# Optimization experiments

Hardware: AMD Instinct MI355X
Metric: run time of the kernel (lower is better)

The kernel has to match this reference:

```python
import jax, jax.numpy as jnp
import numpy as np

N = 8192
COUP = 0.08
ALPHA = 0.45
DT = 0.01
DIFF = 10.0


def setup_inputs() -> dict:
    key = jax.random.key(0)
    k1, k2, k3 = jax.random.split(key, 3)
    phase = jax.random.normal(k1, (N,), dtype=jnp.float32)
    w = jax.random.uniform(k2, (N,), dtype=jnp.float32) * (2.0 * np.pi * 1.5)
    xy = jax.random.normal(k3, (N, 2), dtype=jnp.float32) * 0.05
    xy_dot_old = jnp.zeros((N, 2), dtype=jnp.float32)
    return {"phase": phase, "w": w, "xy": xy, "xy_dot_old": xy_dot_old}


def reference(phase, w, xy, xy_dot_old):
    n = xy.shape[0]
    x = xy[:, 0]
    y = xy[:, 1]

    # per-edge rotation R(d_ij) with d_ij = phase_i - phase_j; diagonal d_ii = 0 -> R = I
    d = phase[:, None] - phase[None, :]            # (n, n)
    c = jnp.cos(d)
    s = jnp.sin(d)

    # sum_j R_ij @ xy_j over ALL j (diagonal contributes identity * xy_i),
    # then remove the self term since adjacency excludes i == j.
    sum_x = c @ x - s @ y                          # (n,)
    sum_y = s @ x + c @ y
    inv_deg = 1.0 / (n - 1)
    coup_x = COUP * (sum_x - x) * inv_deg
    coup_y = COUP * (sum_y - y) * inv_deg

    # local Hopf-like dynamics
    r2 = x * x + y * y
    a = ALPHA * (1.0 - r2)
    xdot = a * x - w * y + coup_x
    ydot = w * x + a * y + coup_y

    # slew-rate clamp to old derivative +/- DIFF
    xdot = jnp.clip(xdot, xy_dot_old[:, 0] - DIFF, xy_dot_old[:, 0] + DIFF)
    ydot = jnp.clip(ydot, xy_dot_old[:, 1] - DIFF, xy_dot_old[:, 1] + DIFF)

    new_xyd = jnp.stack([xdot, ydot], axis=-1)     # (n, 2)
    new_xy = xy + DT * new_xyd                     # (n, 2)
    y_unit = jnp.clip(new_xy[:, 1], -1.0, 1.0)     # unit outputs in [-1, 1]
    return new_xy, new_xyd, y_unit
```

## Files before the change

kernel.cpp:

```cpp
#include <hip/hip_runtime.h>
#include <math.h>


#define NOSC 8192
#define NTHREADS 1024
#define PER_THREAD (NOSC / NTHREADS)

__global__ __launch_bounds__(NTHREADS, 1) void nacpg_kernel(
    const float* __restrict__ phase,
    const float* __restrict__ w,
    const float* __restrict__ xy,
    const float* __restrict__ xy_dot_old,
    float* __restrict__ out)
{
    constexpr float COUP  = 0.08f;
    constexpr float ALPHA = 0.45f;
    constexpr float DT    = 0.01f;
    constexpr float DIFF  = 10.0f;

    const int tid = threadIdx.x;

    float c[PER_THREAD], s[PER_THREAD], x[PER_THREAD], y[PER_THREAD];
    float sA = 0.f, sB = 0.f, sC = 0.f, sD = 0.f;

    #pragma unroll
    for (int k = 0; k < PER_THREAD; ++k) {
        const int i = tid + k * NTHREADS;
        const float p = phase[i];
        const float2 v = reinterpret_cast<const float2*>(xy)[i];
        x[k] = v.x; y[k] = v.y;
        float ss, cc;
        sincosf(p, &ss, &cc);
        c[k] = cc; s[k] = ss;
        sA = fmaf(cc, v.x, sA);
        sB = fmaf(ss, v.x, sB);
        sC = fmaf(cc, v.y, sC);
        sD = fmaf(ss, v.y, sD);
    }

    #pragma unroll
    for (int off = 32; off >= 1; off >>= 1) {
        sA += __shfl_xor(sA, off);
        sB += __shfl_xor(sB, off);
        sC += __shfl_xor(sC, off);
        sD += __shfl_xor(sD, off);
    }

    __shared__ float red[4][NTHREADS / 64];
    const int wave = tid >> 6;
    const int lane = tid & 63;
    if (lane == 0) {
        red[0][wave] = sA; red[1][wave] = sB;
        red[2][wave] = sC; red[3][wave] = sD;
    }
    __syncthreads();

    float A = 0.f, B = 0.f, C = 0.f, D = 0.f;
    #pragma unroll
    for (int wv = 0; wv < NTHREADS / 64; ++wv) {
        A += red[0][wv]; B += red[1][wv];
        C += red[2][wv]; D += red[3][wv];
    }

    const float AD = A + D;
    const float BC = B - C;
    const float CB = C - B;
    const float inv_deg = 1.0f / (float)(NOSC - 1);

    float2* __restrict__ out_xy  = reinterpret_cast<float2*>(out);
    float2* __restrict__ out_xyd = reinterpret_cast<float2*>(out + 2 * NOSC);
    float*  __restrict__ out_yu  = out + 4 * NOSC;

    #pragma unroll
    for (int k = 0; k < PER_THREAD; ++k) {
        const int i = tid + k * NTHREADS;
        const float ci = c[k], si = s[k];
        const float xi = x[k], yi = y[k];

        const float sum_x = ci * AD + si * BC;
        const float sum_y = si * AD + ci * CB;
        const float coup_x = COUP * (sum_x - xi) * inv_deg;
        const float coup_y = COUP * (sum_y - yi) * inv_deg;

        const float r2 = xi * xi + yi * yi;
        const float a  = ALPHA * (1.0f - r2);
        const float wi = w[i];

        float xdot = a * xi - wi * yi + coup_x;
        float ydot = wi * xi + a * yi + coup_y;

        const float2 old = reinterpret_cast<const float2*>(xy_dot_old)[i];
        xdot = fminf(fmaxf(xdot, old.x - DIFF), old.x + DIFF);
        ydot = fminf(fmaxf(ydot, old.y - DIFF), old.y + DIFF);

        const float nx = xi + DT * xdot;
        const float ny = yi + DT * ydot;

        out_xy[i]  = make_float2(nx, ny);
        out_xyd[i] = make_float2(xdot, ydot);
        out_yu[i]  = fminf(fmaxf(ny, -1.0f), 1.0f);
    }
}

extern "C" void kernel_launch(void* const* d_in, const int* in_sizes, int n_in,
                              void* d_out, int out_size, void* d_ws, size_t ws_size,
                              hipStream_t stream) {
    const float* phase      = (const float*)d_in[0];
    const float* w          = (const float*)d_in[1];
    const float* xy         = (const float*)d_in[2];
    const float* xy_dot_old = (const float*)d_in[3];
    float* out = (float*)d_out;

    nacpg_kernel<<<1, NTHREADS, 0, stream>>>(phase, w, xy, xy_dot_old, out);
}
```

Baseline: 64.79 us.

## Split into two multi-block kernels with workspace partial sums and fast sincos

Replaces the single 1024-thread block with two launches of 64 blocks each. The first kernel computes per-block partial sums of cos/sin-weighted x and y into workspace. The second kernel reduces the 64 partials in every wave and computes the per-oscillator update. It also switches to the fast __sincosf intrinsic, which can lose accuracy for large phase arguments, and adds a second launch's overhead.

```diff
diff --git a/kernel.cpp b/kernel.cpp
--- a/kernel.cpp
+++ b/kernel.cpp
@@ -3,14 +3,50 @@
 
 
 #define NOSC 8192
-#define NTHREADS 1024
-#define PER_THREAD (NOSC / NTHREADS)
+#define NTHR 128
+#define NBLK (NOSC / NTHR)
 
-__global__ __launch_bounds__(NTHREADS, 1) void nacpg_kernel(
+__global__ __launch_bounds__(NTHR, 1) void nacpg_partial(
+    const float* __restrict__ phase,
+    const float* __restrict__ xy,
+    float4* __restrict__ part)
+{
+    const int i = blockIdx.x * NTHR + threadIdx.x;
+    const float p = phase[i];
+    const float2 v = reinterpret_cast<const float2*>(xy)[i];
+    float s, c;
+    __sincosf(p, &s, &c);
+
+    float A = c * v.x;
+    float B = s * v.x;
+    float C = c * v.y;
+    float D = s * v.y;
+
+    #pragma unroll
+    for (int off = 32; off >= 1; off >>= 1) {
+        A += __shfl_xor(A, off);
+        B += __shfl_xor(B, off);
+        C += __shfl_xor(C, off);
+        D += __shfl_xor(D, off);
+    }
+
+    __shared__ float4 red[NTHR / 64];
+    const int wave = threadIdx.x >> 6;
+    const int lane = threadIdx.x & 63;
+    if (lane == 0) red[wave] = make_float4(A, B, C, D);
+    __syncthreads();
+    if (threadIdx.x == 0) {
+        float4 a = red[0], b = red[1];
+        part[blockIdx.x] = make_float4(a.x + b.x, a.y + b.y, a.z + b.z, a.w + b.w);
+    }
+}
+
+__global__ __launch_bounds__(NTHR, 1) void nacpg_main(
     const float* __restrict__ phase,
     const float* __restrict__ w,
     const float* __restrict__ xy,
     const float* __restrict__ xy_dot_old,
+    const float4* __restrict__ part,
     float* __restrict__ out)
 {
     constexpr float COUP  = 0.08f;
@@ -18,48 +54,22 @@
     constexpr float DT    = 0.01f;
     constexpr float DIFF  = 10.0f;
 
-    const int tid = threadIdx.x;
+    const int i    = blockIdx.x * NTHR + threadIdx.x;
+    const int lane = threadIdx.x & 63;
 
-    float c[PER_THREAD], s[PER_THREAD], x[PER_THREAD], y[PER_THREAD];
-    float sA = 0.f, sB = 0.f, sC = 0.f, sD = 0.f;
+    const float p       = phase[i];
+    const float wi      = w[i];
+    const float2 v      = reinterpret_cast<const float2*>(xy)[i];
+    const float2 old    = reinterpret_cast<const float2*>(xy_dot_old)[i];
 
-    #pragma unroll
-    for (int k = 0; k < PER_THREAD; ++k) {
-        const int i = tid + k * NTHREADS;
-        const float p = phase[i];
-        const float2 v = reinterpret_cast<const float2*>(xy)[i];
-        x[k] = v.x; y[k] = v.y;
-        float ss, cc;
-        sincosf(p, &ss, &cc);
-        c[k] = cc; s[k] = ss;
-        sA = fmaf(cc, v.x, sA);
-        sB = fmaf(ss, v.x, sB);
-        sC = fmaf(cc, v.y, sC);
-        sD = fmaf(ss, v.y, sD);
-    }
-
+    float4 pp = part[lane];
+    float A = pp.x, B = pp.y, C = pp.z, D = pp.w;
     #pragma unroll
     for (int off = 32; off >= 1; off >>= 1) {
-        sA += __shfl_xor(sA, off);
-        sB += __shfl_xor(sB, off);
-        sC += __shfl_xor(sC, off);
-        sD += __shfl_xor(sD, off);
-    }
-
-    __shared__ float red[4][NTHREADS / 64];
-    const int wave = tid >> 6;
-    const int lane = tid & 63;
-    if (lane == 0) {
-        red[0][wave] = sA; red[1][wave] = sB;
-        red[2][wave] = sC; red[3][wave] = sD;
-    }
-    __syncthreads();
-
-    float A = 0.f, B = 0.f, C = 0.f, D = 0.f;
-    #pragma unroll
-    for (int wv = 0; wv < NTHREADS / 64; ++wv) {
-        A += red[0][wv]; B += red[1][wv];
-        C += red[2][wv]; D += red[3][wv];
+        A += __shfl_xor(A, off);
+        B += __shfl_xor(B, off);
+        C += __shfl_xor(C, off);
+        D += __shfl_xor(D, off);
     }
 
     const float AD = A + D;
@@ -67,39 +77,30 @@
     const float CB = C - B;
     const float inv_deg = 1.0f / (float)(NOSC - 1);
 
-    float2* __restrict__ out_xy  = reinterpret_cast<float2*>(out);
-    float2* __restrict__ out_xyd = reinterpret_cast<float2*>(out + 2 * NOSC);
-    float*  __restrict__ out_yu  = out + 4 * NOSC;
+    float s, c;
+    __sincosf(p, &s, &c);
 
-    #pragma unroll
-    for (int k = 0; k < PER_THREAD; ++k) {
-        const int i = tid + k * NTHREADS;
-        const float ci = c[k], si = s[k];
-        const float xi = x[k], yi = y[k];
+    const float xi = v.x, yi = v.y;
+    const float sum_x = c * AD + s * BC;
+    const float sum_y = s * AD + c * CB;
+    const float coup_x = COUP * (sum_x - xi) * inv_deg;
+    const float coup_y = COUP * (sum_y - yi) * inv_deg;
 
-        const float sum_x = ci * AD + si * BC;
-        const float sum_y = si * AD + ci * CB;
-        const float coup_x = COUP * (sum_x - xi) * inv_deg;
-        const float coup_y = COUP * (sum_y - yi) * inv_deg;
+    const float r2 = xi * xi + yi * yi;
+    const float a  = ALPHA * (1.0f - r2);
 
-        const float r2 = xi * xi + yi * yi;
-        const float a  = ALPHA * (1.0f - r2);
-        const float wi = w[i];
+    float xdot = a * xi - wi * yi + coup_x;
+    float ydot = wi * xi + a * yi + coup_y;
 
-        float xdot = a * xi - wi * yi + coup_x;
-        float ydot = wi * xi + a * yi + coup_y;
+    xdot = fminf(fmaxf(xdot, old.x - DIFF), old.x + DIFF);
+    ydot = fminf(fmaxf(ydot, old.y - DIFF), old.y + DIFF);
 
-        const float2 old = reinterpret_cast<const float2*>(xy_dot_old)[i];
-        xdot = fminf(fmaxf(xdot, old.x - DIFF), old.x + DIFF);
-        ydot = fminf(fmaxf(ydot, old.y - DIFF), old.y + DIFF);
+    const float nx = xi + DT * xdot;
+    const float ny = yi + DT * ydot;
 
-        const float nx = xi + DT * xdot;
-        const float ny = yi + DT * ydot;
-
-        out_xy[i]  = make_float2(nx, ny);
-        out_xyd[i] = make_float2(xdot, ydot);
-        out_yu[i]  = fminf(fmaxf(ny, -1.0f), 1.0f);
-    }
+    reinterpret_cast<float2*>(out)[i]             = make_float2(nx, ny);
+    reinterpret_cast<float2*>(out + 2 * NOSC)[i]  = make_float2(xdot, ydot);
+    out[4 * NOSC + i] = fminf(fmaxf(ny, -1.0f), 1.0f);
 }
 
 extern "C" void kernel_launch(void* const* d_in, const int* in_sizes, int n_in,
@@ -109,7 +110,9 @@
     const float* w          = (const float*)d_in[1];
     const float* xy         = (const float*)d_in[2];
     const float* xy_dot_old = (const float*)d_in[3];
-    float* out = (float*)d_out;
+    float* out   = (float*)d_out;
+    float4* part = (float4*)d_ws;
 
-    nacpg_kernel<<<1, NTHREADS, 0, stream>>>(phase, w, xy, xy_dot_old, out);
+    nacpg_partial<<<NBLK, NTHR, 0, stream>>>(phase, xy, part);
+    nacpg_main<<<NBLK, NTHR, 0, stream>>>(phase, w, xy, xy_dot_old, part, out);
 }
```

After: 61.34 us. -5.3%, faster.
